# Optimization experiments

Measured on AMD Instinct MI355X. Metric: run time of the kernel, lower is better.

## Reference

```python
import jax, jax.numpy as jnp
import numpy as np

NUM_HEADS = 16
NUM_KV_HEADS = 8
HEAD_DIM = 64
SCALE = 0.125  # 1/sqrt(64)
GROUP = NUM_HEADS // NUM_KV_HEADS
BATCH = 4
SEQ_LEN = 1024
T = BATCH * SEQ_LEN          # total flattened tokens
NUM_SLOTS = 8192             # paged KV-cache slots (num_blocks * block_size)


def setup_inputs() -> dict:
    key = jax.random.key(0)
    kq, kk, kv, kp = jax.random.split(key, 4)
    q = jax.random.normal(kq, (T, NUM_HEADS * HEAD_DIM), dtype=jnp.float32)
    k = jax.random.normal(kk, (T, NUM_KV_HEADS * HEAD_DIM), dtype=jnp.float32)
    v = jax.random.normal(kv, (T, NUM_KV_HEADS * HEAD_DIM), dtype=jnp.float32)
    k_cache = jnp.zeros((NUM_SLOTS, NUM_KV_HEADS * HEAD_DIM), dtype=jnp.float32)
    v_cache = jnp.zeros((NUM_SLOTS, NUM_KV_HEADS * HEAD_DIM), dtype=jnp.float32)
    # irregular (permuted) slot assignment, vLLM-style paged layout
    slot_mapping = jax.random.permutation(kp, NUM_SLOTS)[:T].astype(jnp.int32)
    cu_seqlens = (jnp.arange(BATCH + 1, dtype=jnp.int32) * SEQ_LEN)
    return {"q": q, "k": k, "v": v, "k_cache": k_cache, "v_cache": v_cache,
            "slot_mapping": slot_mapping, "cu_seqlens": cu_seqlens}


def reference(q, k, v, k_cache, v_cache, slot_mapping, cu_seqlens):
    # --- store_kvcache: scatter new K/V rows into paged caches ---
    k_cache = k_cache.at[slot_mapping].set(k)
    v_cache = v_cache.at[slot_mapping].set(v)

    # prefill-with-block-tables path: K/V are read back from the cache
    kh = k_cache[slot_mapping].reshape(T, NUM_KV_HEADS, HEAD_DIM)
    vh = v_cache[slot_mapping].reshape(T, NUM_KV_HEADS, HEAD_DIM)
    qh = q.reshape(T, NUM_KV_HEADS, GROUP, HEAD_DIM)  # GQA grouping

    # varlen causal mask from cu_seqlens: attend iff same sequence and j <= i
    idx = jnp.arange(T)
    seg = jnp.searchsorted(cu_seqlens, idx, side='right')  # sequence id per token
    mask = (seg[:, None] == seg[None, :]) & (idx[:, None] >= idx[None, :])  # [T,T]

    scores = jnp.einsum('tkgd,skd->kgts', qh, kh) * SCALE  # [Hk,G,T,T]
    scores = jnp.where(mask, scores, -jnp.inf)
    w = jax.nn.softmax(scores, axis=-1)
    o = jnp.einsum('kgts,skd->tkgd', w, vh).reshape(T, NUM_HEADS * HEAD_DIM)
    return o
```

## Files before the change

kernel.cpp:

```cpp
#include <hip/hip_runtime.h>
#include <hip/hip_bf16.h>

typedef __attribute__((ext_vector_type(4))) float  f32x4;
typedef __attribute__((ext_vector_type(8))) short  bf16x8;
typedef __attribute__((ext_vector_type(4))) short  bf16x4;

constexpr int SEQ  = 1024;
constexpr float SC = 0.125f * 1.44269504088896340736f;

#define SWZ(row, bcol) ((((row) * 128) + (bcol)) ^ (((row) & 7) << 4))

#define TRREAD(dst, addr, IMM) \
    asm volatile("ds_read_b64_tr_b16 %0, %1 offset:%c2" : "=v"(dst) : "v"(addr), "n"(IMM))

__device__ __forceinline__ short f2bfn(float x) {
    return __builtin_bit_cast(short, __float2bfloat16(x));
}

template<int CTRL>
__device__ __forceinline__ float dppf(float x) {
    return __builtin_bit_cast(float,
        __builtin_amdgcn_mov_dpp(__builtin_bit_cast(int, x), CTRL, 0xF, 0xF, true));
}
__device__ __forceinline__ float rowmax16(float x) {
    x = fmaxf(x, dppf<0xB1>(x));
    x = fmaxf(x, dppf<0x4E>(x));
    x = fmaxf(x, dppf<0x124>(x));
    x = fmaxf(x, dppf<0x128>(x));
    return x;
}
__device__ __forceinline__ float rowsum16(float x) {
    x += dppf<0xB1>(x);
    x += dppf<0x4E>(x);
    x += dppf<0x124>(x);
    x += dppf<0x128>(x);
    return x;
}

__global__ __launch_bounds__(512, 4)
void attn_fwd(const float* __restrict__ q,
              const float* __restrict__ k,
              const float* __restrict__ v,
              float* __restrict__ out)
{
    __shared__ char smem[49152];

    const int bid = blockIdx.x;
    const int hi2 = bid >> 8;
    const int ii  = bid & 255;
    const int bh  = ii >> 3;
    const int t   = ii & 7;
    const int qt  = hi2 ? (15 - t) : t;
    const int b   = bh >> 3;
    const int kh  = bh & 7;

    const int tid = threadIdx.x;
    const int l   = tid & 63;
    const int w   = tid >> 6;
    const int e   = w >> 2;
    const int wq  = w & 3;
    const int lg  = l >> 4;
    const int ll  = l & 15;

    char* Pb = smem + 32768 + w * 2048;

    const int dk = lg * 8;
    const float* qb = q + (size_t)(b * SEQ + qt * 64 + wq * 16 + ll) * 1024 + (2 * kh + e) * 64;
    f32x4 q0 = *(const f32x4*)(qb + dk);
    f32x4 q1 = *(const f32x4*)(qb + dk + 4);
    f32x4 q2 = *(const f32x4*)(qb + dk + 32);
    f32x4 q3 = *(const f32x4*)(qb + dk + 36);
    bf16x8 qa0, qa1;
    #pragma unroll
    for (int i = 0; i < 4; ++i) {
        qa0[i]     = f2bfn(q0[i] * SC);
        qa0[i + 4] = f2bfn(q1[i] * SC);
        qa1[i]     = f2bfn(q2[i] * SC);
        qa1[i + 4] = f2bfn(q3[i] * SC);
    }

    f32x4 acc[4] = {};
    float mrow[4] = {-INFINITY, -INFINITY, -INFINITY, -INFINITY};
    float lrow[4] = {0.f, 0.f, 0.f, 0.f};

    const int st   = tid & 255;
    const int srow = st >> 2;
    const int scol = (st & 3) * 16;
    const float* gsrc = (e ? v : k) + (size_t)(b * SEQ + srow) * 512 + kh * 64 + scol;
    unsigned sdo0, sdo1;
    if (e == 0) {
        sdo0 = SWZ(srow, scol * 2);
        sdo1 = SWZ(srow, scol * 2 + 16);
    } else {
        sdo0 = ((srow >> 2) * 4 + (scol >> 4)) * 128 + (srow & 3) * 32;
        sdo1 = sdo0 + 16;
    }
    char* sbase = smem + (e ? 16384 : 0);

    const unsigned vtr0 = (unsigned)(size_t)(smem + 16384) + lg * 1024 + ll * 8;

    f32x4 pre0 = *(const f32x4*)(gsrc);
    f32x4 pre1 = *(const f32x4*)(gsrc + 4);
    f32x4 pre2 = *(const f32x4*)(gsrc + 8);
    f32x4 pre3 = *(const f32x4*)(gsrc + 12);
    {
        bf16x8 h0, h1;
        #pragma unroll
        for (int i = 0; i < 4; ++i) {
            h0[i] = f2bfn(pre0[i]); h0[i + 4] = f2bfn(pre1[i]);
            h1[i] = f2bfn(pre2[i]); h1[i + 4] = f2bfn(pre3[i]);
        }
        *(bf16x8*)(sbase + sdo0) = h0;
        *(bf16x8*)(sbase + sdo1) = h1;
    }
    __syncthreads();

    for (int kvb = 0; kvb <= qt; ++kvb) {
        const int cur = kvb & 1;
        char* Kc = smem + cur * 8192;
        const unsigned vtrc = vtr0 + cur * 8192;

        if (kvb < qt) {
            const float* g = gsrc + (size_t)(kvb + 1) * (64 * 512);
            pre0 = *(const f32x4*)(g);
            pre1 = *(const f32x4*)(g + 4);
            pre2 = *(const f32x4*)(g + 8);
            pre3 = *(const f32x4*)(g + 12);
        }

        f32x4 s_[4] = {};
        #pragma unroll
        for (int c = 0; c < 4; ++c) {
            const int krow = c * 16 + ll;
            bf16x8 kb0 = *(const bf16x8*)(Kc + SWZ(krow, dk * 2));
            bf16x8 kb1 = *(const bf16x8*)(Kc + SWZ(krow, (dk + 32) * 2));
            s_[c] = __builtin_amdgcn_mfma_f32_16x16x32_bf16(qa0, kb0, s_[c], 0, 0, 0);
            s_[c] = __builtin_amdgcn_mfma_f32_16x16x32_bf16(qa1, kb1, s_[c], 0, 0, 0);
        }

        if (kvb == qt) {
            #pragma unroll
            for (int c = 0; c < 4; ++c) {
                const int col = c * 16 + ll;
                #pragma unroll
                for (int j = 0; j < 4; ++j) {
                    const int row = wq * 16 + lg * 4 + j;
                    if (col > row) s_[c][j] = -INFINITY;
                }
            }
        }

        #pragma unroll
        for (int j = 0; j < 4; ++j) {
            float mx = fmaxf(fmaxf(s_[0][j], s_[1][j]), fmaxf(s_[2][j], s_[3][j]));
            mx = rowmax16(mx);
            float nm = fmaxf(mrow[j], mx);
            float fj = __builtin_amdgcn_exp2f(mrow[j] - nm);
            mrow[j] = nm;
            float sum = 0.f;
            #pragma unroll
            for (int c = 0; c < 4; ++c) {
                float p = __builtin_amdgcn_exp2f(s_[c][j] - nm);
                sum += p;
                *(unsigned short*)(Pb + SWZ(lg * 4 + j, (c * 16 + ll) * 2)) = (unsigned short)f2bfn(p);
            }
            sum = rowsum16(sum);
            lrow[j] = lrow[j] * fj + sum;
            #pragma unroll
            for (int dc = 0; dc < 4; ++dc) acc[dc][j] *= fj;
        }

#define PV_KC(KCOFF, kc) { \
        bf16x8 pa = *(const bf16x8*)(Pb + SWZ(ll, (kc) * 64 + lg * 16)); \
        bf16x4 t00, t01, t10, t11, t20, t21, t30, t31; \
        TRREAD(t00, vtrc, KCOFF + 0);   TRREAD(t01, vtrc, KCOFF + 512); \
        TRREAD(t10, vtrc, KCOFF + 128); TRREAD(t11, vtrc, KCOFF + 640); \
        TRREAD(t20, vtrc, KCOFF + 256); TRREAD(t21, vtrc, KCOFF + 768); \
        TRREAD(t30, vtrc, KCOFF + 384); TRREAD(t31, vtrc, KCOFF + 896); \
        asm volatile("s_waitcnt lgkmcnt(0)" ::: "memory"); \
        __builtin_amdgcn_sched_barrier(0); \
        bf16x8 vb0 = __builtin_shufflevector(t00, t01, 0, 1, 2, 3, 4, 5, 6, 7); \
        bf16x8 vb1 = __builtin_shufflevector(t10, t11, 0, 1, 2, 3, 4, 5, 6, 7); \
        bf16x8 vb2 = __builtin_shufflevector(t20, t21, 0, 1, 2, 3, 4, 5, 6, 7); \
        bf16x8 vb3 = __builtin_shufflevector(t30, t31, 0, 1, 2, 3, 4, 5, 6, 7); \
        acc[0] = __builtin_amdgcn_mfma_f32_16x16x32_bf16(pa, vb0, acc[0], 0, 0, 0); \
        acc[1] = __builtin_amdgcn_mfma_f32_16x16x32_bf16(pa, vb1, acc[1], 0, 0, 0); \
        acc[2] = __builtin_amdgcn_mfma_f32_16x16x32_bf16(pa, vb2, acc[2], 0, 0, 0); \
        acc[3] = __builtin_amdgcn_mfma_f32_16x16x32_bf16(pa, vb3, acc[3], 0, 0, 0); \
    }
        PV_KC(0, 0);
        PV_KC(4096, 1);
#undef PV_KC

        if (kvb < qt) {
            bf16x8 h0, h1;
            #pragma unroll
            for (int i = 0; i < 4; ++i) {
                h0[i] = f2bfn(pre0[i]); h0[i + 4] = f2bfn(pre1[i]);
                h1[i] = f2bfn(pre2[i]); h1[i + 4] = f2bfn(pre3[i]);
            }
            char* sb = sbase + (cur ^ 1) * 8192;
            *(bf16x8*)(sb + sdo0) = h0;
            *(bf16x8*)(sb + sdo1) = h1;
        }
        __syncthreads();
    }

    #pragma unroll
    for (int j = 0; j < 4; ++j) {
        float inv = 1.f / lrow[j];
        const int rowg = qt * 64 + wq * 16 + lg * 4 + j;
        float* ob = out + (size_t)(b * SEQ + rowg) * 1024 + (2 * kh + e) * 64;
        #pragma unroll
        for (int dc = 0; dc < 4; ++dc)
            ob[dc * 16 + ll] = acc[dc][j] * inv;
    }
}

extern "C" void kernel_launch(void* const* d_in, const int* in_sizes, int n_in,
                              void* d_out, int out_size, void* d_ws, size_t ws_size,
                              hipStream_t stream) {
    const float* q = (const float*)d_in[0];
    const float* k = (const float*)d_in[1];
    const float* v = (const float*)d_in[2];
    float* out = (float*)d_out;

    attn_fwd<<<dim3(512), dim3(512), 0, stream>>>(q, k, v, out);
}
```

Baseline: 126.7 us.

## Process two KV tiles per iteration with independent softmax streams

The loop now stages two 64-row K/V tiles into shared memory per iteration, with LDS grown to 64KB. Each wave runs two independent online-softmax accumulators (A and B) on alternating tiles and merges them at the end with a log-sum-exp rescale. The aim is to halve the number of block barriers and give the MFMA and exp work two independent dependency chains for more instruction-level parallelism. The cost is more register pressure, larger LDS per block, and a wasted duplicate load when the tile count is odd.

```diff
diff --git a/kernel.cpp b/kernel.cpp
--- a/kernel.cpp
+++ b/kernel.cpp
@@ -43,7 +43,7 @@
               const float* __restrict__ v,
               float* __restrict__ out)
 {
-    __shared__ char smem[49152];
+    __shared__ char smem[65536];
 
     const int bid = blockIdx.x;
     const int hi2 = bid >> 8;
@@ -62,7 +62,8 @@
     const int lg  = l >> 4;
     const int ll  = l & 15;
 
-    char* Pb = smem + 32768 + w * 2048;
+    char* PbA = smem + 32768 + w * 4096;
+    char* PbB = PbA + 2048;
 
     const int dk = lg * 8;
     const float* qb = q + (size_t)(b * SEQ + qt * 64 + wq * 16 + ll) * 1024 + (2 * kh + e) * 64;
@@ -79,141 +80,146 @@
         qa1[i + 4] = f2bfn(q3[i] * SC);
     }
 
-    f32x4 acc[4] = {};
-    float mrow[4] = {-INFINITY, -INFINITY, -INFINITY, -INFINITY};
-    float lrow[4] = {0.f, 0.f, 0.f, 0.f};
-
+    f32x4 accA[4] = {}, accB[4] = {};
+    float mA[4] = {-INFINITY, -INFINITY, -INFINITY, -INFINITY};
+    float mB[4] = {-INFINITY, -INFINITY, -INFINITY, -INFINITY};
+    float lA[4] = {}, lB[4] = {};
+
+    const int e2   = tid >> 8;
     const int st   = tid & 255;
     const int srow = st >> 2;
     const int scol = (st & 3) * 16;
-    const float* gsrc = (e ? v : k) + (size_t)(b * SEQ + srow) * 512 + kh * 64 + scol;
+    const float* gsrc = (e2 ? v : k) + (size_t)(b * SEQ + srow) * 512 + kh * 64 + scol;
     unsigned sdo0, sdo1;
-    if (e == 0) {
+    char* sb0;
+    if (e2 == 0) {
         sdo0 = SWZ(srow, scol * 2);
         sdo1 = SWZ(srow, scol * 2 + 16);
+        sb0  = smem;
     } else {
         sdo0 = ((srow >> 2) * 4 + (scol >> 4)) * 128 + (srow & 3) * 32;
         sdo1 = sdo0 + 16;
-    }
-    char* sbase = smem + (e ? 16384 : 0);
-
-    const unsigned vtr0 = (unsigned)(size_t)(smem + 16384) + lg * 1024 + ll * 8;
-
-    f32x4 pre0 = *(const f32x4*)(gsrc);
-    f32x4 pre1 = *(const f32x4*)(gsrc + 4);
-    f32x4 pre2 = *(const f32x4*)(gsrc + 8);
-    f32x4 pre3 = *(const f32x4*)(gsrc + 12);
-    {
-        bf16x8 h0, h1;
-        #pragma unroll
-        for (int i = 0; i < 4; ++i) {
-            h0[i] = f2bfn(pre0[i]); h0[i + 4] = f2bfn(pre1[i]);
-            h1[i] = f2bfn(pre2[i]); h1[i + 4] = f2bfn(pre3[i]);
-        }
-        *(bf16x8*)(sbase + sdo0) = h0;
-        *(bf16x8*)(sbase + sdo1) = h1;
-    }
-    __syncthreads();
-
-    for (int kvb = 0; kvb <= qt; ++kvb) {
-        const int cur = kvb & 1;
-        char* Kc = smem + cur * 8192;
-        const unsigned vtrc = vtr0 + cur * 8192;
-
-        if (kvb < qt) {
-            const float* g = gsrc + (size_t)(kvb + 1) * (64 * 512);
-            pre0 = *(const f32x4*)(g);
-            pre1 = *(const f32x4*)(g + 4);
-            pre2 = *(const f32x4*)(g + 8);
-            pre3 = *(const f32x4*)(g + 12);
-        }
-
-        f32x4 s_[4] = {};
-        #pragma unroll
-        for (int c = 0; c < 4; ++c) {
-            const int krow = c * 16 + ll;
-            bf16x8 kb0 = *(const bf16x8*)(Kc + SWZ(krow, dk * 2));
-            bf16x8 kb1 = *(const bf16x8*)(Kc + SWZ(krow, (dk + 32) * 2));
-            s_[c] = __builtin_amdgcn_mfma_f32_16x16x32_bf16(qa0, kb0, s_[c], 0, 0, 0);
-            s_[c] = __builtin_amdgcn_mfma_f32_16x16x32_bf16(qa1, kb1, s_[c], 0, 0, 0);
-        }
-
-        if (kvb == qt) {
+        sb0  = smem + 16384;
+    }
+
+    const unsigned vtrA = (unsigned)(size_t)(smem + 16384) + lg * 1024 + ll * 8;
+    const unsigned vtrB = vtrA + 8192;
+
+    const int n     = qt + 1;
+    const int iters = (n + 1) >> 1;
+
+    f32x4 pA0, pA1, pA2, pA3, pB0, pB1, pB2, pB3;
+#define LOADT(I) { \
+        const float* gA = gsrc + (size_t)(2 * (I)) * (64 * 512); \
+        const float* gB = gsrc + (size_t)(((2 * (I) + 1) < qt) ? (2 * (I) + 1) : qt) * (64 * 512); \
+        pA0 = *(const f32x4*)(gA);     pA1 = *(const f32x4*)(gA + 4); \
+        pA2 = *(const f32x4*)(gA + 8); pA3 = *(const f32x4*)(gA + 12); \
+        pB0 = *(const f32x4*)(gB);     pB1 = *(const f32x4*)(gB + 4); \
+        pB2 = *(const f32x4*)(gB + 8); pB3 = *(const f32x4*)(gB + 12); \
+    }
+
+    LOADT(0);
+
+    for (int i = 0; i < iters; ++i) {
+        __syncthreads();
+        {
+            bf16x8 h0, h1, h2, h3;
             #pragma unroll
-            for (int c = 0; c < 4; ++c) {
-                const int col = c * 16 + ll;
-                #pragma unroll
-                for (int j = 0; j < 4; ++j) {
-                    const int row = wq * 16 + lg * 4 + j;
-                    if (col > row) s_[c][j] = -INFINITY;
-                }
+            for (int x = 0; x < 4; ++x) {
+                h0[x] = f2bfn(pA0[x]); h0[x + 4] = f2bfn(pA1[x]);
+                h1[x] = f2bfn(pA2[x]); h1[x + 4] = f2bfn(pA3[x]);
+                h2[x] = f2bfn(pB0[x]); h2[x + 4] = f2bfn(pB1[x]);
+                h3[x] = f2bfn(pB2[x]); h3[x + 4] = f2bfn(pB3[x]);
             }
-        }
-
-        #pragma unroll
-        for (int j = 0; j < 4; ++j) {
-            float mx = fmaxf(fmaxf(s_[0][j], s_[1][j]), fmaxf(s_[2][j], s_[3][j]));
-            mx = rowmax16(mx);
-            float nm = fmaxf(mrow[j], mx);
-            float fj = __builtin_amdgcn_exp2f(mrow[j] - nm);
-            mrow[j] = nm;
-            float sum = 0.f;
-            #pragma unroll
-            for (int c = 0; c < 4; ++c) {
-                float p = __builtin_amdgcn_exp2f(s_[c][j] - nm);
-                sum += p;
-                *(unsigned short*)(Pb + SWZ(lg * 4 + j, (c * 16 + ll) * 2)) = (unsigned short)f2bfn(p);
-            }
-            sum = rowsum16(sum);
-            lrow[j] = lrow[j] * fj + sum;
-            #pragma unroll
-            for (int dc = 0; dc < 4; ++dc) acc[dc][j] *= fj;
-        }
-
-#define PV_KC(KCOFF, kc) { \
-        bf16x8 pa = *(const bf16x8*)(Pb + SWZ(ll, (kc) * 64 + lg * 16)); \
-        bf16x4 t00, t01, t10, t11, t20, t21, t30, t31; \
-        TRREAD(t00, vtrc, KCOFF + 0);   TRREAD(t01, vtrc, KCOFF + 512); \
-        TRREAD(t10, vtrc, KCOFF + 128); TRREAD(t11, vtrc, KCOFF + 640); \
-        TRREAD(t20, vtrc, KCOFF + 256); TRREAD(t21, vtrc, KCOFF + 768); \
-        TRREAD(t30, vtrc, KCOFF + 384); TRREAD(t31, vtrc, KCOFF + 896); \
-        asm volatile("s_waitcnt lgkmcnt(0)" ::: "memory"); \
-        __builtin_amdgcn_sched_barrier(0); \
-        bf16x8 vb0 = __builtin_shufflevector(t00, t01, 0, 1, 2, 3, 4, 5, 6, 7); \
-        bf16x8 vb1 = __builtin_shufflevector(t10, t11, 0, 1, 2, 3, 4, 5, 6, 7); \
-        bf16x8 vb2 = __builtin_shufflevector(t20, t21, 0, 1, 2, 3, 4, 5, 6, 7); \
-        bf16x8 vb3 = __builtin_shufflevector(t30, t31, 0, 1, 2, 3, 4, 5, 6, 7); \
-        acc[0] = __builtin_amdgcn_mfma_f32_16x16x32_bf16(pa, vb0, acc[0], 0, 0, 0); \
-        acc[1] = __builtin_amdgcn_mfma_f32_16x16x32_bf16(pa, vb1, acc[1], 0, 0, 0); \
-        acc[2] = __builtin_amdgcn_mfma_f32_16x16x32_bf16(pa, vb2, acc[2], 0, 0, 0); \
-        acc[3] = __builtin_amdgcn_mfma_f32_16x16x32_bf16(pa, vb3, acc[3], 0, 0, 0); \
-    }
-        PV_KC(0, 0);
-        PV_KC(4096, 1);
-#undef PV_KC
-
-        if (kvb < qt) {
-            bf16x8 h0, h1;
-            #pragma unroll
-            for (int i = 0; i < 4; ++i) {
-                h0[i] = f2bfn(pre0[i]); h0[i + 4] = f2bfn(pre1[i]);
-                h1[i] = f2bfn(pre2[i]); h1[i + 4] = f2bfn(pre3[i]);
-            }
-            char* sb = sbase + (cur ^ 1) * 8192;
-            *(bf16x8*)(sb + sdo0) = h0;
-            *(bf16x8*)(sb + sdo1) = h1;
+            *(bf16x8*)(sb0 + sdo0)        = h0;
+            *(bf16x8*)(sb0 + sdo1)        = h1;
+            *(bf16x8*)(sb0 + 8192 + sdo0) = h2;
+            *(bf16x8*)(sb0 + 8192 + sdo1) = h3;
         }
         __syncthreads();
+
+        if (i + 1 < iters) LOADT(i + 1);
+
+        const int maskA = (2 * i == qt);
+        const int haveB = (2 * i + 1 <= qt);
+        const int maskB = (2 * i + 1 == qt);
+
+#define TILE(KBASE, VTR, PB, ACC, Mv, Lv, DOMASK) { \
+        f32x4 s_[4] = {}; \
+        _Pragma("unroll") \
+        for (int c = 0; c < 4; ++c) { \
+            const int krow = c * 16 + ll; \
+            bf16x8 kb0 = *(const bf16x8*)((KBASE) + SWZ(krow, dk * 2)); \
+            bf16x8 kb1 = *(const bf16x8*)((KBASE) + SWZ(krow, (dk + 32) * 2)); \
+            s_[c] = __builtin_amdgcn_mfma_f32_16x16x32_bf16(qa0, kb0, s_[c], 0, 0, 0); \
+            s_[c] = __builtin_amdgcn_mfma_f32_16x16x32_bf16(qa1, kb1, s_[c], 0, 0, 0); \
+        } \
+        if (DOMASK) { \
+            _Pragma("unroll") \
+            for (int c = 0; c < 4; ++c) { \
+                const int col = c * 16 + ll; \
+                _Pragma("unroll") \
+                for (int j = 0; j < 4; ++j) \
+                    if (col > wq * 16 + lg * 4 + j) s_[c][j] = -INFINITY; \
+            } \
+        } \
+        _Pragma("unroll") \
+        for (int j = 0; j < 4; ++j) { \
+            float mx = fmaxf(fmaxf(s_[0][j], s_[1][j]), fmaxf(s_[2][j], s_[3][j])); \
+            mx = rowmax16(mx); \
+            float nm = fmaxf(Mv[j], mx); \
+            float fj = __builtin_amdgcn_exp2f(Mv[j] - nm); \
+            Mv[j] = nm; \
+            float sum = 0.f; \
+            _Pragma("unroll") \
+            for (int c = 0; c < 4; ++c) { \
+                float p = __builtin_amdgcn_exp2f(s_[c][j] - nm); \
+                sum += p; \
+                *(unsigned short*)((PB) + SWZ(lg * 4 + j, (c * 16 + ll) * 2)) = (unsigned short)f2bfn(p); \
+            } \
+            sum = rowsum16(sum); \
+            Lv[j] = Lv[j] * fj + sum; \
+            _Pragma("unroll") \
+            for (int dc = 0; dc < 4; ++dc) ACC[dc][j] *= fj; \
+        } \
+        _Pragma("unroll") \
+        for (int kc = 0; kc < 2; ++kc) { \
+            bf16x8 pa = *(const bf16x8*)((PB) + SWZ(ll, kc * 64 + lg * 16)); \
+            const unsigned vr = (VTR) + kc * 4096; \
+            bf16x4 t00, t01, t10, t11, t20, t21, t30, t31; \
+            TRREAD(t00, vr, 0);   TRREAD(t01, vr, 512); \
+            TRREAD(t10, vr, 128); TRREAD(t11, vr, 640); \
+            TRREAD(t20, vr, 256); TRREAD(t21, vr, 768); \
+            TRREAD(t30, vr, 384); TRREAD(t31, vr, 896); \
+            asm volatile("s_waitcnt lgkmcnt(0)" ::: "memory"); \
+            __builtin_amdgcn_sched_barrier(0); \
+            bf16x8 vb0 = __builtin_shufflevector(t00, t01, 0, 1, 2, 3, 4, 5, 6, 7); \
+            bf16x8 vb1 = __builtin_shufflevector(t10, t11, 0, 1, 2, 3, 4, 5, 6, 7); \
+            bf16x8 vb2 = __builtin_shufflevector(t20, t21, 0, 1, 2, 3, 4, 5, 6, 7); \
+            bf16x8 vb3 = __builtin_shufflevector(t30, t31, 0, 1, 2, 3, 4, 5, 6, 7); \
+            ACC[0] = __builtin_amdgcn_mfma_f32_16x16x32_bf16(pa, vb0, ACC[0], 0, 0, 0); \
+            ACC[1] = __builtin_amdgcn_mfma_f32_16x16x32_bf16(pa, vb1, ACC[1], 0, 0, 0); \
+            ACC[2] = __builtin_amdgcn_mfma_f32_16x16x32_bf16(pa, vb2, ACC[2], 0, 0, 0); \
+            ACC[3] = __builtin_amdgcn_mfma_f32_16x16x32_bf16(pa, vb3, ACC[3], 0, 0, 0); \
+        } \
+    }
+
+        TILE(smem,        vtrA, PbA, accA, mA, lA, maskA);
+        if (haveB) TILE(smem + 8192, vtrB, PbB, accB, mB, lB, maskB);
+#undef TILE
     }
 
     #pragma unroll
     for (int j = 0; j < 4; ++j) {
-        float inv = 1.f / lrow[j];
+        float m  = fmaxf(mA[j], mB[j]);
+        float aA = __builtin_amdgcn_exp2f(mA[j] - m);
+        float aB = __builtin_amdgcn_exp2f(mB[j] - m);
+        float inv = 1.f / (lA[j] * aA + lB[j] * aB);
         const int rowg = qt * 64 + wq * 16 + lg * 4 + j;
         float* ob = out + (size_t)(b * SEQ + rowg) * 1024 + (2 * kh + e) * 64;
         #pragma unroll
         for (int dc = 0; dc < 4; ++dc)
-            ob[dc * 16 + ll] = acc[dc][j] * inv;
+            ob[dc * 16 + ll] = (accA[dc][j] * aA + accB[dc][j] * aB) * inv;
     }
 }
 
```

Result: slower. 204.9 us (+61.7%).

## Split KV range across two wave groups per block and merge softmax partials

Applied to the files above, without the earlier changes.

Each block now covers 32 query rows instead of 64, doubling the grid. Within a block, two groups of four waves each process half of the causal KV tiles, with K and V for both halves staged together. Their online-softmax partial states (max, sum, accumulator) are merged through shared memory at the end. The aim is to shorten the serial KV loop of long-row tiles and improve load balance, at the cost of more shared memory (80KB, which likely limits blocks per CU), extra global reloads of K/V across the doubled grid, and a merge step.

```diff
diff --git a/kernel.cpp b/kernel.cpp
--- a/kernel.cpp
+++ b/kernel.cpp
@@ -43,29 +43,36 @@
               const float* __restrict__ v,
               float* __restrict__ out)
 {
-    __shared__ char smem[49152];
+    __shared__ char smem[81920];
 
     const int bid = blockIdx.x;
-    const int hi2 = bid >> 8;
+    const int z   = bid >> 8;
     const int ii  = bid & 255;
     const int bh  = ii >> 3;
     const int t   = ii & 7;
-    const int qt  = hi2 ? (15 - t) : t;
+    const int qt  = (z & 1) ? (15 - t) : t;
+    const int rh  = z >> 1;
     const int b   = bh >> 3;
     const int kh  = bh & 7;
 
     const int tid = threadIdx.x;
     const int l   = tid & 63;
     const int w   = tid >> 6;
-    const int e   = w >> 2;
-    const int wq  = w & 3;
     const int lg  = l >> 4;
     const int ll  = l & 15;
-
-    char* Pb = smem + 32768 + w * 2048;
+    const int wl  = w & 3;
+    const int e   = wl >> 1;
+    const int rg  = wl & 1;
+    const int ck  = w >> 2;
+
+    const int h   = (qt >> 1) + 1;
+    const int c1  = (qt + 1) >> 1;
+    const int maskI = ck ? (c1 - 1) : qt;
+
+    char* Pb = smem + 65536 + w * 2048;
 
     const int dk = lg * 8;
-    const float* qb = q + (size_t)(b * SEQ + qt * 64 + wq * 16 + ll) * 1024 + (2 * kh + e) * 64;
+    const float* qb = q + (size_t)(b * SEQ + qt * 64 + rh * 32 + rg * 16 + ll) * 1024 + (2 * kh + e) * 64;
     f32x4 q0 = *(const f32x4*)(qb + dk);
     f32x4 q1 = *(const f32x4*)(qb + dk + 4);
     f32x4 q2 = *(const f32x4*)(qb + dk + 32);
@@ -83,137 +90,165 @@
     float mrow[4] = {-INFINITY, -INFINITY, -INFINITY, -INFINITY};
     float lrow[4] = {0.f, 0.f, 0.f, 0.f};
 
+    const int role = tid >> 8;
     const int st   = tid & 255;
     const int srow = st >> 2;
     const int scol = (st & 3) * 16;
-    const float* gsrc = (e ? v : k) + (size_t)(b * SEQ + srow) * 512 + kh * 64 + scol;
+    const float* gsrc = (role ? v : k) + (size_t)(b * SEQ + srow) * 512 + kh * 64 + scol;
     unsigned sdo0, sdo1;
-    if (e == 0) {
+    if (role == 0) {
         sdo0 = SWZ(srow, scol * 2);
         sdo1 = SWZ(srow, scol * 2 + 16);
     } else {
         sdo0 = ((srow >> 2) * 4 + (scol >> 4)) * 128 + (srow & 3) * 32;
         sdo1 = sdo0 + 16;
     }
-    char* sbase = smem + (e ? 16384 : 0);
-
-    const unsigned vtr0 = (unsigned)(size_t)(smem + 16384) + lg * 1024 + ll * 8;
-
-    f32x4 pre0 = *(const f32x4*)(gsrc);
-    f32x4 pre1 = *(const f32x4*)(gsrc + 4);
-    f32x4 pre2 = *(const f32x4*)(gsrc + 8);
-    f32x4 pre3 = *(const f32x4*)(gsrc + 12);
-    {
-        bf16x8 h0, h1;
-        #pragma unroll
-        for (int i = 0; i < 4; ++i) {
-            h0[i] = f2bfn(pre0[i]); h0[i + 4] = f2bfn(pre1[i]);
-            h1[i] = f2bfn(pre2[i]); h1[i + 4] = f2bfn(pre3[i]);
+    char* sbase = smem + (role ? 32768 : 0);
+
+    const unsigned vtrb = (unsigned)(size_t)smem + 32768 + (ck << 14) + lg * 1024 + ll * 8;
+    char* kbase0 = smem + (ck << 14);
+
+    f32x4 pA0, pA1, pA2, pA3, pB0, pB1, pB2, pB3;
+#define LOADT(I) { \
+        const float* gA = gsrc + (size_t)(I) * 32768; \
+        int _ib = ((I) < c1) ? (I) : (c1 ? c1 - 1 : 0); \
+        const float* gB = gsrc + (size_t)(h + _ib) * 32768; \
+        pA0 = *(const f32x4*)(gA);     pA1 = *(const f32x4*)(gA + 4); \
+        pA2 = *(const f32x4*)(gA + 8); pA3 = *(const f32x4*)(gA + 12); \
+        pB0 = *(const f32x4*)(gB);     pB1 = *(const f32x4*)(gB + 4); \
+        pB2 = *(const f32x4*)(gB + 8); pB3 = *(const f32x4*)(gB + 12); \
+    }
+#define STAGE(BUF) { \
+        bf16x8 h0, h1, h2, h3; \
+        _Pragma("unroll") \
+        for (int x = 0; x < 4; ++x) { \
+            h0[x] = f2bfn(pA0[x]); h0[x + 4] = f2bfn(pA1[x]); \
+            h1[x] = f2bfn(pA2[x]); h1[x + 4] = f2bfn(pA3[x]); \
+            h2[x] = f2bfn(pB0[x]); h2[x + 4] = f2bfn(pB1[x]); \
+            h3[x] = f2bfn(pB2[x]); h3[x + 4] = f2bfn(pB3[x]); \
+        } \
+        char* sb = sbase + (BUF) * 8192; \
+        *(bf16x8*)(sb + sdo0)         = h0; \
+        *(bf16x8*)(sb + sdo1)         = h1; \
+        *(bf16x8*)(sb + 16384 + sdo0) = h2; \
+        *(bf16x8*)(sb + 16384 + sdo1) = h3; \
+    }
+
+    LOADT(0);
+    STAGE(0);
+    __syncthreads();
+
+    for (int i = 0; i < h; ++i) {
+        const int cur = i & 1;
+        const int more = (i + 1 < h);
+        if (more) LOADT(i + 1);
+
+        const int valid = (ck == 0) | (i < c1);
+        if (valid) {
+            char* Kc = kbase0 + cur * 8192;
+            const unsigned vtr = vtrb + cur * 8192;
+
+            f32x4 s_[4] = {};
+            #pragma unroll
+            for (int c = 0; c < 4; ++c) {
+                const int krow = c * 16 + ll;
+                bf16x8 kb0 = *(const bf16x8*)(Kc + SWZ(krow, dk * 2));
+                bf16x8 kb1 = *(const bf16x8*)(Kc + SWZ(krow, (dk + 32) * 2));
+                s_[c] = __builtin_amdgcn_mfma_f32_16x16x32_bf16(qa0, kb0, s_[c], 0, 0, 0);
+                s_[c] = __builtin_amdgcn_mfma_f32_16x16x32_bf16(qa1, kb1, s_[c], 0, 0, 0);
+            }
+
+            if (i == maskI) {
+                #pragma unroll
+                for (int c = 0; c < 4; ++c) {
+                    const int col = c * 16 + ll;
+                    #pragma unroll
+                    for (int j = 0; j < 4; ++j)
+                        if (col > rh * 32 + rg * 16 + lg * 4 + j) s_[c][j] = -INFINITY;
+                }
+            }
+
+            #pragma unroll
+            for (int j = 0; j < 4; ++j) {
+                float mx = fmaxf(fmaxf(s_[0][j], s_[1][j]), fmaxf(s_[2][j], s_[3][j]));
+                mx = rowmax16(mx);
+                float nm = fmaxf(mrow[j], mx);
+                float fj = __builtin_amdgcn_exp2f(mrow[j] - nm);
+                mrow[j] = nm;
+                float sum = 0.f;
+                #pragma unroll
+                for (int c = 0; c < 4; ++c) {
+                    float p = __builtin_amdgcn_exp2f(s_[c][j] - nm);
+                    sum += p;
+                    *(unsigned short*)(Pb + SWZ(lg * 4 + j, (c * 16 + ll) * 2)) = (unsigned short)f2bfn(p);
+                }
+                sum = rowsum16(sum);
+                lrow[j] = lrow[j] * fj + sum;
+                #pragma unroll
+                for (int dc = 0; dc < 4; ++dc) acc[dc][j] *= fj;
+            }
+
+            #pragma unroll
+            for (int kc = 0; kc < 2; ++kc) {
+                bf16x8 pa = *(const bf16x8*)(Pb + SWZ(ll, kc * 64 + lg * 16));
+                const unsigned vr = vtr + kc * 4096;
+                bf16x4 t00, t01, t10, t11, t20, t21, t30, t31;
+                TRREAD(t00, vr, 0);   TRREAD(t01, vr, 512);
+                TRREAD(t10, vr, 128); TRREAD(t11, vr, 640);
+                TRREAD(t20, vr, 256); TRREAD(t21, vr, 768);
+                TRREAD(t30, vr, 384); TRREAD(t31, vr, 896);
+                asm volatile("s_waitcnt lgkmcnt(0)" ::: "memory");
+                __builtin_amdgcn_sched_barrier(0);
+                bf16x8 vb0 = __builtin_shufflevector(t00, t01, 0, 1, 2, 3, 4, 5, 6, 7);
+                bf16x8 vb1 = __builtin_shufflevector(t10, t11, 0, 1, 2, 3, 4, 5, 6, 7);
+                bf16x8 vb2 = __builtin_shufflevector(t20, t21, 0, 1, 2, 3, 4, 5, 6, 7);
+                bf16x8 vb3 = __builtin_shufflevector(t30, t31, 0, 1, 2, 3, 4, 5, 6, 7);
+                acc[0] = __builtin_amdgcn_mfma_f32_16x16x32_bf16(pa, vb0, acc[0], 0, 0, 0);
+                acc[1] = __builtin_amdgcn_mfma_f32_16x16x32_bf16(pa, vb1, acc[1], 0, 0, 0);
+                acc[2] = __builtin_amdgcn_mfma_f32_16x16x32_bf16(pa, vb2, acc[2], 0, 0, 0);
+                acc[3] = __builtin_amdgcn_mfma_f32_16x16x32_bf16(pa, vb3, acc[3], 0, 0, 0);
+            }
         }
-        *(bf16x8*)(sbase + sdo0) = h0;
-        *(bf16x8*)(sbase + sdo1) = h1;
+
+        if (more) STAGE(cur ^ 1);
+        __syncthreads();
+    }
+#undef LOADT
+#undef STAGE
+
+    if (ck) {
+        char* mb = smem + (w - 4) * 6144 + l * 96;
+        f32x4 mv = {mrow[0], mrow[1], mrow[2], mrow[3]};
+        f32x4 lv = {lrow[0], lrow[1], lrow[2], lrow[3]};
+        *(f32x4*)(mb)      = mv;
+        *(f32x4*)(mb + 16) = lv;
+        *(f32x4*)(mb + 32) = acc[0];
+        *(f32x4*)(mb + 48) = acc[1];
+        *(f32x4*)(mb + 64) = acc[2];
+        *(f32x4*)(mb + 80) = acc[3];
     }
     __syncthreads();
-
-    for (int kvb = 0; kvb <= qt; ++kvb) {
-        const int cur = kvb & 1;
-        char* Kc = smem + cur * 8192;
-        const unsigned vtrc = vtr0 + cur * 8192;
-
-        if (kvb < qt) {
-            const float* g = gsrc + (size_t)(kvb + 1) * (64 * 512);
-            pre0 = *(const f32x4*)(g);
-            pre1 = *(const f32x4*)(g + 4);
-            pre2 = *(const f32x4*)(g + 8);
-            pre3 = *(const f32x4*)(g + 12);
-        }
-
-        f32x4 s_[4] = {};
-        #pragma unroll
-        for (int c = 0; c < 4; ++c) {
-            const int krow = c * 16 + ll;
-            bf16x8 kb0 = *(const bf16x8*)(Kc + SWZ(krow, dk * 2));
-            bf16x8 kb1 = *(const bf16x8*)(Kc + SWZ(krow, (dk + 32) * 2));
-            s_[c] = __builtin_amdgcn_mfma_f32_16x16x32_bf16(qa0, kb0, s_[c], 0, 0, 0);
-            s_[c] = __builtin_amdgcn_mfma_f32_16x16x32_bf16(qa1, kb1, s_[c], 0, 0, 0);
-        }
-
-        if (kvb == qt) {
-            #pragma unroll
-            for (int c = 0; c < 4; ++c) {
-                const int col = c * 16 + ll;
-                #pragma unroll
-                for (int j = 0; j < 4; ++j) {
-                    const int row = wq * 16 + lg * 4 + j;
-                    if (col > row) s_[c][j] = -INFINITY;
-                }
-            }
-        }
-
+    if (!ck) {
+        char* mb = smem + w * 6144 + l * 96;
+        f32x4 mBv = *(const f32x4*)(mb);
+        f32x4 lBv = *(const f32x4*)(mb + 16);
+        f32x4 aB[4];
+        aB[0] = *(const f32x4*)(mb + 32);
+        aB[1] = *(const f32x4*)(mb + 48);
+        aB[2] = *(const f32x4*)(mb + 64);
+        aB[3] = *(const f32x4*)(mb + 80);
         #pragma unroll
         for (int j = 0; j < 4; ++j) {
-            float mx = fmaxf(fmaxf(s_[0][j], s_[1][j]), fmaxf(s_[2][j], s_[3][j]));
-            mx = rowmax16(mx);
-            float nm = fmaxf(mrow[j], mx);
-            float fj = __builtin_amdgcn_exp2f(mrow[j] - nm);
-            mrow[j] = nm;
-            float sum = 0.f;
-            #pragma unroll
-            for (int c = 0; c < 4; ++c) {
-                float p = __builtin_amdgcn_exp2f(s_[c][j] - nm);
-                sum += p;
-                *(unsigned short*)(Pb + SWZ(lg * 4 + j, (c * 16 + ll) * 2)) = (unsigned short)f2bfn(p);
-            }
-            sum = rowsum16(sum);
-            lrow[j] = lrow[j] * fj + sum;
-            #pragma unroll
-            for (int dc = 0; dc < 4; ++dc) acc[dc][j] *= fj;
+            float m  = fmaxf(mrow[j], mBv[j]);
+            float fA = __builtin_amdgcn_exp2f(mrow[j] - m);
+            float fB = __builtin_amdgcn_exp2f(mBv[j] - m);
+            float inv = 1.f / (lrow[j] * fA + lBv[j] * fB);
+            const int rowg = qt * 64 + rh * 32 + rg * 16 + lg * 4 + j;
+            float* ob = out + (size_t)(b * SEQ + rowg) * 1024 + (2 * kh + e) * 64;
+            #pragma unroll
+            for (int dc = 0; dc < 4; ++dc)
+                ob[dc * 16 + ll] = (acc[dc][j] * fA + aB[dc][j] * fB) * inv;
         }
-
-#define PV_KC(KCOFF, kc) { \
-        bf16x8 pa = *(const bf16x8*)(Pb + SWZ(ll, (kc) * 64 + lg * 16)); \
-        bf16x4 t00, t01, t10, t11, t20, t21, t30, t31; \
-        TRREAD(t00, vtrc, KCOFF + 0);   TRREAD(t01, vtrc, KCOFF + 512); \
-        TRREAD(t10, vtrc, KCOFF + 128); TRREAD(t11, vtrc, KCOFF + 640); \
-        TRREAD(t20, vtrc, KCOFF + 256); TRREAD(t21, vtrc, KCOFF + 768); \
-        TRREAD(t30, vtrc, KCOFF + 384); TRREAD(t31, vtrc, KCOFF + 896); \
-        asm volatile("s_waitcnt lgkmcnt(0)" ::: "memory"); \
-        __builtin_amdgcn_sched_barrier(0); \
-        bf16x8 vb0 = __builtin_shufflevector(t00, t01, 0, 1, 2, 3, 4, 5, 6, 7); \
-        bf16x8 vb1 = __builtin_shufflevector(t10, t11, 0, 1, 2, 3, 4, 5, 6, 7); \
-        bf16x8 vb2 = __builtin_shufflevector(t20, t21, 0, 1, 2, 3, 4, 5, 6, 7); \
-        bf16x8 vb3 = __builtin_shufflevector(t30, t31, 0, 1, 2, 3, 4, 5, 6, 7); \
-        acc[0] = __builtin_amdgcn_mfma_f32_16x16x32_bf16(pa, vb0, acc[0], 0, 0, 0); \
-        acc[1] = __builtin_amdgcn_mfma_f32_16x16x32_bf16(pa, vb1, acc[1], 0, 0, 0); \
-        acc[2] = __builtin_amdgcn_mfma_f32_16x16x32_bf16(pa, vb2, acc[2], 0, 0, 0); \
-        acc[3] = __builtin_amdgcn_mfma_f32_16x16x32_bf16(pa, vb3, acc[3], 0, 0, 0); \
-    }
-        PV_KC(0, 0);
-        PV_KC(4096, 1);
-#undef PV_KC
-
-        if (kvb < qt) {
-            bf16x8 h0, h1;
-            #pragma unroll
-            for (int i = 0; i < 4; ++i) {
-                h0[i] = f2bfn(pre0[i]); h0[i + 4] = f2bfn(pre1[i]);
-                h1[i] = f2bfn(pre2[i]); h1[i + 4] = f2bfn(pre3[i]);
-            }
-            char* sb = sbase + (cur ^ 1) * 8192;
-            *(bf16x8*)(sb + sdo0) = h0;
-            *(bf16x8*)(sb + sdo1) = h1;
-        }
-        __syncthreads();
-    }
-
-    #pragma unroll
-    for (int j = 0; j < 4; ++j) {
-        float inv = 1.f / lrow[j];
-        const int rowg = qt * 64 + wq * 16 + lg * 4 + j;
-        float* ob = out + (size_t)(b * SEQ + rowg) * 1024 + (2 * kh + e) * 64;
-        #pragma unroll
-        for (int dc = 0; dc < 4; ++dc)
-            ob[dc * 16 + ll] = acc[dc][j] * inv;
     }
 }
 
@@ -225,5 +260,5 @@
     const float* v = (const float*)d_in[2];
     float* out = (float*)d_out;
 
-    attn_fwd<<<dim3(512), dim3(512), 0, stream>>>(q, k, v, out);
-}
+    attn_fwd<<<dim3(1024), dim3(512), 0, stream>>>(q, k, v, out);
+}
```

New measurement: 150.4 us. +18.7%, slower.
